# Kernel optimization log

Measured on AMD Instinct MI355X. Metric: run time of the kernel, lower is better.

Reference implementation:

```python
import jax, jax.numpy as jnp
import numpy as np
from jax import lax

B, S, F, H, V, T = 64, 1024, 128, 512, 64, 64
SOS, EOS = 0, 1


def lstm_cell(x, h, c, W_ih, W_hh, b_ih, b_hh):
    # PyTorch LSTM gate order: i, f, g, o
    gates = x @ W_ih.T + h @ W_hh.T + b_ih + b_hh  # [B, 4H]
    i, f, g, o = jnp.split(gates, 4, axis=-1)
    c_new = jax.nn.sigmoid(f) * c + jax.nn.sigmoid(i) * jnp.tanh(g)
    h_new = jax.nn.sigmoid(o) * jnp.tanh(c_new)
    return h_new, c_new


def setup_inputs() -> dict:
    key = jax.random.key(0)
    ks = jax.random.split(key, 12)
    s = 0.05  # weight scale to avoid gate saturation
    return {
        "signal": jax.random.normal(ks[0], (B, S, F), jnp.float32),
        "target": jax.random.randint(ks[1], (B, T), 0, V),
        "enc_W_ih": jax.random.normal(ks[2], (4 * H, F), jnp.float32) * s,
        "enc_W_hh": jax.random.normal(ks[3], (4 * H, H), jnp.float32) * s,
        "enc_b_ih": jax.random.normal(ks[4], (4 * H,), jnp.float32) * s,
        "enc_b_hh": jax.random.normal(ks[5], (4 * H,), jnp.float32) * s,
        "dec_W_ih": jax.random.normal(ks[6], (4 * H, V), jnp.float32) * s,
        "dec_W_hh": jax.random.normal(ks[7], (4 * H, H), jnp.float32) * s,
        "dec_b_ih": jax.random.normal(ks[8], (4 * H,), jnp.float32) * s,
        "dec_b_hh": jax.random.normal(ks[9], (4 * H,), jnp.float32) * s,
        "out_W": jax.random.normal(ks[10], (V, H), jnp.float32) * s,
        "out_b": jax.random.normal(ks[11], (V,), jnp.float32) * s,
    }


def reference(signal, target, enc_W_ih, enc_W_hh, enc_b_ih, enc_b_hh,
              dec_W_ih, dec_W_hh, dec_b_ih, dec_b_hh, out_W, out_b):
    b = signal.shape[0]
    hdim = enc_W_hh.shape[1]
    vocab = out_b.shape[0]
    n_steps = target.shape[1]  # max_loop = target.size(1)

    # ---- encoder LSTM (only final hidden state is used downstream) ----
    def enc_step(carry, x_t):
        h, c = carry
        h, c = lstm_cell(x_t, h, c, enc_W_ih, enc_W_hh, enc_b_ih, enc_b_hh)
        return (h, c), None

    h0 = jnp.zeros((b, hdim), signal.dtype)
    (h, c), _ = lax.scan(enc_step, (h0, h0), jnp.swapaxes(signal, 0, 1))

    # ---- decoder: teacher-start (one-hot target[:,0]) then greedy feedback ----
    inp0 = jax.nn.one_hot(target[:, 0], vocab, dtype=signal.dtype)  # [B, V]

    def dec_step(carry, _):
        h, c, x = carry
        x = jax.nn.relu(x)  # F.relu on one-hot input (faithful to source)
        h, c = lstm_cell(x, h, c, dec_W_ih, dec_W_hh, dec_b_ih, dec_b_hh)
        logits = h @ out_W.T + out_b  # [B, V]
        nxt = jax.nn.one_hot(jnp.argmax(logits, axis=-1), vocab, dtype=x.dtype)
        return (h, c, nxt), logits

    (_, _, _), logits = lax.scan(dec_step, (h, c, inp0), None, length=n_steps)
    logits = jnp.swapaxes(logits, 0, 1)  # [B, T, V]
    return jax.nn.log_softmax(logits, axis=-1)
```

## Files before the change

kernel.cpp:

```cpp
#include <hip/hip_runtime.h>
#include <cstddef>
#include <math.h>

#define NGROUP 4
#define WPG    32
#define NWG    128
#define BPG    16
#define BB  64
#define HH  512
#define TT  64
#define VV  64
#define FF  128
#define SS  1024

typedef _Float16 f16;
typedef _Float16 f16x8 __attribute__((ext_vector_type(8)));
typedef float    f32x4 __attribute__((ext_vector_type(4)));
typedef unsigned int u32;
typedef u32 u32x2 __attribute__((ext_vector_type(2)));
typedef u32 u32x4 __attribute__((ext_vector_type(4)));
typedef unsigned long long u64;

#define C1 4.8828125e-4f
#define C2 2.384185791015625e-7f

__device__ __forceinline__ void split8(const float* __restrict__ p, f16x8& hi, f16x8& lo) {
  f32x4 u = *(const f32x4*)p;
  f32x4 v = *(const f32x4*)(p + 4);
#pragma unroll
  for (int j = 0; j < 4; ++j) {
    f16 a = (f16)u[j]; hi[j]   = a; lo[j]   = (f16)((u[j] - (float)a) * 2048.0f);
    f16 b = (f16)v[j]; hi[4+j] = b; lo[4+j] = (f16)((v[j] - (float)b) * 2048.0f);
  }
}
__device__ __forceinline__ float sigmf_(float x) { return 1.0f / (1.0f + expf(-x)); }

__device__ __forceinline__ f32x4 ld16f(const void* p) {
  f32x4 r;
  asm volatile("global_load_dwordx4 %0, %1, off sc0 sc1" : "=v"(r) : "v"(p) : "memory");
  return r;
}
__device__ __forceinline__ void st4f(u32* p, u32 v) {
  __hip_atomic_store(p, v, __ATOMIC_RELAXED, __HIP_MEMORY_SCOPE_AGENT);
}
__device__ __forceinline__ void st4ff(float* p, float v) {
  __hip_atomic_store(p, v, __ATOMIC_RELAXED, __HIP_MEMORY_SCOPE_AGENT);
}
__device__ __forceinline__ u32 ld4f(const u32* p) {
  return __hip_atomic_load(p, __ATOMIC_RELAXED, __HIP_MEMORY_SCOPE_AGENT);
}
#define VMWAIT asm volatile("s_waitcnt vmcnt(0)" ::: "memory")

__device__ __forceinline__ void wait_flags(const u32* flags, u32 target, int lane) {
  const u32* a = flags + (size_t)(lane & 31) * 32;
  while (!__all(ld4f(a) >= target))
    __builtin_amdgcn_s_sleep(1);
}

#define MFMA(d, a, b) d = __builtin_amdgcn_mfma_f32_16x16x32_f16(a, b, d, 0, 0, 0)

#define STAGE_H(src_)                                                         \
  { const u32* src = (src_) + (size_t)(tid >> 4) * HH;                        \
    const int cq_ = tid & 15;                                                 \
    f32x4 sv[8];                                                              \
    _Pragma("unroll") for (int u2 = 0; u2 < 8; ++u2)                          \
      sv[u2] = ld16f(src + cq_*4 + u2*64);                                    \
    VMWAIT;                                                                   \
    _Pragma("unroll") for (int u2 = 0; u2 < 8; ++u2)                          \
      asm volatile("" : "+v"(sv[u2]));                                        \
    __builtin_amdgcn_sched_barrier(0);                                        \
    const int r_ = tid >> 4;                                                  \
    const size_t swz = (size_t)((r_ & 7) << 4);                               \
    _Pragma("unroll") for (int u2 = 0; u2 < 8; ++u2) {                        \
      union { f32x4 f; u32 u4[4]; } U; U.f = sv[u2];                          \
      u32 h0_ = (U.u4[0] & 0xffffu) | (U.u4[1] << 16);                        \
      u32 h1_ = (U.u4[2] & 0xffffu) | (U.u4[3] << 16);                        \
      u32 l0_ = (U.u4[0] >> 16) | (U.u4[1] & 0xffff0000u);                    \
      u32 l1_ = (U.u4[2] >> 16) | (U.u4[3] & 0xffff0000u);                    \
      size_t off = ((size_t)r_*1024 + (size_t)cq_*8 + (size_t)u2*128) ^ swz;  \
      *(u32x2*)((char*)sh_hi + off) = (u32x2){h0_, h1_};                      \
      *(u32x2*)((char*)sh_lo + off) = (u32x2){l0_, l1_};                      \
    } }                                                                       \
  __syncthreads();

#define LDA(s, ah, al)                                                        \
  { size_t o_ = ((size_t)mn * 1024 + (size_t)(s) * 64 + (size_t)(q8 * 2))     \
                ^ (size_t)((mn & 7) << 4);                                    \
    ah = *(const f16x8*)((const char*)sh_hi + o_);                            \
    al = *(const f16x8*)((const char*)sh_lo + o_); }

#define HPART()                                                               \
  _Pragma("unroll") for (int s = 0; s < 16; ++s) {                            \
    f16x8 ah, al; LDA(s, ah, al);                                             \
    MFMA(acc0, ah, whh_h[s]);                                                 \
    MFMA(acc1, al, whh_h[s]);                                                 \
    MFMA(acc1, ah, whh_l[s]);                                                 \
    MFMA(acc2, al, whh_l[s]);                                                 \
  }

#define GWRITE()                                                              \
  _Pragma("unroll") for (int r = 0; r < 4; ++r)                               \
    gate_buf[w][q * 4 + r][mn] = acc0[r] + C1 * acc1[r] + C2 * acc2[r];

__global__ void __launch_bounds__(256, 1) lstm_seq2seq(
    const float* __restrict__ sig,
    const int*   __restrict__ tgt,
    const float* __restrict__ eWih,
    const float* __restrict__ eWhh,
    const float* __restrict__ eBih,
    const float* __restrict__ eBhh,
    const float* __restrict__ dWih,
    const float* __restrict__ dWhh,
    const float* __restrict__ dBih,
    const float* __restrict__ dBhh,
    const float* __restrict__ oW,
    const float* __restrict__ oB,
    float*       __restrict__ out,
    unsigned char* __restrict__ ws)
{
  const int wg = blockIdx.x;
  const int g  = wg >> 5;
  const int p  = wg & 31;
  const int gb = g * BPG;
  u32* fl     = (u32*)ws + (size_t)g * 1024;
  u32* idxbuf = (u32*)(ws + 16384);
  u32* h16[2] = { (u32*)(ws + 20480) + (size_t)(g*2 + 0) * 8192,
                  (u32*)(ws + 20480) + (size_t)(g*2 + 1) * 8192 };
  float* hfg  = (float*)(ws + 282624) + (size_t)g * 8192;

  const int tid  = threadIdx.x;
  const int w    = tid >> 6;
  const int lane = tid & 63;
  const int q    = lane >> 4;
  const int mn   = lane & 15;
  const int q8   = q * 8;
  const int row  = w * HH + p * 16 + mn;
  const int cb   = tid >> 4;
  const int ck   = tid & 15;
  const int crow = p * 16 + ck;

  __shared__ __attribute__((aligned(16))) f16 sh_hi[16 * 512];
  __shared__ __attribute__((aligned(16))) f16 sh_lo[16 * 512];
  __shared__ float gate_buf[4][16][17];
  __shared__ float bias_buf[4][16];
  __shared__ __attribute__((aligned(16))) float hrow[512];
  __shared__ double psum[64];

  f16x8 whh_h[16], whh_l[16], wih_h[4], wih_l[4];
#pragma unroll
  for (int s = 0; s < 16; ++s)
    split8(eWhh + (size_t)row * HH + s * 32 + q8, whh_h[s], whh_l[s]);
#pragma unroll
  for (int s = 0; s < 4; ++s)
    split8(eWih + (size_t)row * FF + s * 32 + q8, wih_h[s], wih_l[s]);
  if (tid < 64) {
    int g4 = tid >> 4, kl = tid & 15;
    int r = g4 * HH + p * 16 + kl;
    bias_buf[g4][kl] = eBih[r] + eBhh[r];
  }
  if (p == 0 && tid < BPG)
    st4f(idxbuf + gb + tid, (u32)tgt[(size_t)(gb + tid) * TT]);
  __syncthreads();

  float c_reg = 0.f;
  int cur = 0;
  const f32x4 zero4 = {0.f, 0.f, 0.f, 0.f};

  for (int t = 0; t < SS; ++t) {
    f32x4 acc0 = zero4, acc1 = zero4, acc2 = zero4;
    const float* sb = sig + (size_t)(gb + mn) * (SS * FF) + (size_t)t * FF;
#pragma unroll
    for (int s = 0; s < 4; ++s) {
      f16x8 ah, al;
      split8(sb + s * 32 + q8, ah, al);
      MFMA(acc0, ah, wih_h[s]);
      MFMA(acc1, al, wih_h[s]);
      MFMA(acc1, ah, wih_l[s]);
      MFMA(acc2, al, wih_l[s]);
    }
    wait_flags(fl, (u32)t, lane);
    STAGE_H(h16[cur])
    HPART()
    GWRITE()
    __syncthreads();
    {
      float gi = gate_buf[0][cb][ck] + bias_buf[0][ck];
      float gf = gate_buf[1][cb][ck] + bias_buf[1][ck];
      float gg = gate_buf[2][cb][ck] + bias_buf[2][ck];
      float go = gate_buf[3][cb][ck] + bias_buf[3][ck];
      float c  = sigmf_(gf) * c_reg + sigmf_(gi) * tanhf(gg);
      float h  = sigmf_(go) * tanhf(c);
      c_reg = c;
      f16 hh = (f16)h;
      f16 hl = (f16)((h - (float)hh) * 2048.0f);
      union { f16 h2[2]; u32 u; } pk;
      pk.h2[0] = hh; pk.h2[1] = hl;
      st4f(h16[cur ^ 1] + (size_t)cb * HH + crow, pk.u);
    }
    VMWAIT;
    __syncthreads();
    if (tid == 0) st4f(fl + p * 32, (u32)(t + 1));
    cur ^= 1;
  }

#pragma unroll
  for (int s = 0; s < 16; ++s)
    split8(dWhh + (size_t)row * HH + s * 32 + q8, whh_h[s], whh_l[s]);
  __syncthreads();
  if (tid < 64) {
    int g4 = tid >> 4, kl = tid & 15;
    int r = g4 * HH + p * 16 + kl;
    bias_buf[g4][kl] = dBih[r] + dBhh[r];
  }
  __syncthreads();

  for (int t = 0; t < TT; ++t) {
    wait_flags(fl, (u32)(SS + 2 * t), lane);
    f32x4 acc0 = zero4, acc1 = zero4, acc2 = zero4;
    STAGE_H(h16[cur])
    HPART()
    GWRITE()
    __syncthreads();
    {
      int ib = (int)ld4f(idxbuf + gb + cb);
      float gi = gate_buf[0][cb][ck] + bias_buf[0][ck] + dWih[(size_t)(0*HH + crow) * VV + ib];
      float gf = gate_buf[1][cb][ck] + bias_buf[1][ck] + dWih[(size_t)(1*HH + crow) * VV + ib];
      float gg = gate_buf[2][cb][ck] + bias_buf[2][ck] + dWih[(size_t)(2*HH + crow) * VV + ib];
      float go = gate_buf[3][cb][ck] + bias_buf[3][ck] + dWih[(size_t)(3*HH + crow) * VV + ib];
      float c  = sigmf_(gf) * c_reg + sigmf_(gi) * tanhf(gg);
      float h  = sigmf_(go) * tanhf(c);
      c_reg = c;
      f16 hh = (f16)h;
      f16 hl = (f16)((h - (float)hh) * 2048.0f);
      union { f16 h2[2]; u32 u; } pk;
      pk.h2[0] = hh; pk.h2[1] = hl;
      st4f(h16[cur ^ 1] + (size_t)cb * HH + crow, pk.u);
      st4ff(hfg + (size_t)cb * HH + crow, h);
    }
    VMWAIT;
    __syncthreads();
    if (tid == 0) st4f(fl + p * 32, (u32)(SS + 2 * t + 1));
    int nxt = cur ^ 1;

    wait_flags(fl, (u32)(SS + 2 * t + 1), lane);
    if (p < BPG) {
      if (tid < 128) {
        f32x4 hv = ld16f(hfg + (size_t)p * HH + tid * 4);
        VMWAIT;
        *(f32x4*)&hrow[tid * 4] = hv;
      }
      __syncthreads();
      double acc = 0.0;
      if (w < 2) {
        const float* wr = oW + (size_t)lane * HH + w * 256;
        const float* hr = hrow + w * 256;
#pragma unroll 4
        for (int kc = 0; kc < 64; ++kc) {
          f32x4 hv = *(const f32x4*)(hr + kc * 4);
          f32x4 wv = *(const f32x4*)(wr + kc * 4);
          acc += (double)hv[0]*(double)wv[0] + (double)hv[1]*(double)wv[1]
               + (double)hv[2]*(double)wv[2] + (double)hv[3]*(double)wv[3];
        }
        if (w == 1) psum[lane] = acc;
      }
      __syncthreads();
      if (w == 0) {
        double l = acc + psum[lane] + (double)oB[lane];
        double mx = l; int ai = lane;
#pragma unroll
        for (int o = 32; o > 0; o >>= 1) {
          double om = __shfl_xor(mx, o, 64);
          int    oi = __shfl_xor(ai, o, 64);
          if (om > mx || (om == mx && oi < ai)) { mx = om; ai = oi; }
        }
        double se = exp(l - mx);
#pragma unroll
        for (int o = 32; o > 0; o >>= 1) se += __shfl_xor(se, o, 64);
        double lse = mx + log(se);
        out[((size_t)(gb + p) * TT + t) * VV + lane] = (float)(l - lse);
        if (lane == 0) st4f(idxbuf + gb + p, (u32)ai);
      }
    }
    VMWAIT;
    __syncthreads();
    if (tid == 0) st4f(fl + p * 32, (u32)(SS + 2 * t + 2));
    cur = nxt;
  }
}

extern "C" void kernel_launch(void* const* d_in, const int* in_sizes, int n_in,
                              void* d_out, int out_size, void* d_ws, size_t ws_size,
                              hipStream_t stream) {
  (void)in_sizes; (void)n_in; (void)out_size; (void)ws_size;
  hipMemsetAsync(d_ws, 0, 282624, stream);
  lstm_seq2seq<<<dim3(NWG), dim3(256), 0, stream>>>(
      (const float*)d_in[0],  (const int*)d_in[1],
      (const float*)d_in[2],  (const float*)d_in[3],
      (const float*)d_in[4],  (const float*)d_in[5],
      (const float*)d_in[6],  (const float*)d_in[7],
      (const float*)d_in[8],  (const float*)d_in[9],
      (const float*)d_in[10], (const float*)d_in[11],
      (float*)d_out, (unsigned char*)d_ws);
}
```

Before: 5.351 ms.

## Exchange hidden state as single fp16 and prefetch next input projection

The hidden state is now passed between workgroups as one fp16 value instead of an fp16 hi/lo pair. This halves the global exchange buffer, the LDS staging, and the recurrent MFMA count per step. The input-projection MFMAs for step t+1 are issued right after the h store of step t, so they overlap with the flag barrier wait instead of sitting on the critical path. The cost is lower precision in the recurrent h·W_hh product, which could drift over 1024 encoder steps and flip decoder argmax choices.

```diff
diff --git a/kernel.cpp b/kernel.cpp
--- a/kernel.cpp
+++ b/kernel.cpp
@@ -17,7 +17,6 @@
 typedef _Float16 f16x8 __attribute__((ext_vector_type(8)));
 typedef float    f32x4 __attribute__((ext_vector_type(4)));
 typedef unsigned int u32;
-typedef u32 u32x2 __attribute__((ext_vector_type(2)));
 typedef u32 u32x4 __attribute__((ext_vector_type(4)));
 typedef unsigned long long u64;
 
@@ -60,47 +59,57 @@
 #define MFMA(d, a, b) d = __builtin_amdgcn_mfma_f32_16x16x32_f16(a, b, d, 0, 0, 0)
 
 #define STAGE_H(src_)                                                         \
-  { const u32* src = (src_) + (size_t)(tid >> 4) * HH;                        \
+  { const u32* src = (src_) + (size_t)(tid >> 4) * 256;                       \
     const int cq_ = tid & 15;                                                 \
-    f32x4 sv[8];                                                              \
-    _Pragma("unroll") for (int u2 = 0; u2 < 8; ++u2)                          \
+    f32x4 sv[4];                                                              \
+    _Pragma("unroll") for (int u2 = 0; u2 < 4; ++u2)                          \
       sv[u2] = ld16f(src + cq_*4 + u2*64);                                    \
     VMWAIT;                                                                   \
-    _Pragma("unroll") for (int u2 = 0; u2 < 8; ++u2)                          \
+    _Pragma("unroll") for (int u2 = 0; u2 < 4; ++u2)                          \
       asm volatile("" : "+v"(sv[u2]));                                        \
     __builtin_amdgcn_sched_barrier(0);                                        \
     const int r_ = tid >> 4;                                                  \
     const size_t swz = (size_t)((r_ & 7) << 4);                               \
-    _Pragma("unroll") for (int u2 = 0; u2 < 8; ++u2) {                        \
-      union { f32x4 f; u32 u4[4]; } U; U.f = sv[u2];                          \
-      u32 h0_ = (U.u4[0] & 0xffffu) | (U.u4[1] << 16);                        \
-      u32 h1_ = (U.u4[2] & 0xffffu) | (U.u4[3] << 16);                        \
-      u32 l0_ = (U.u4[0] >> 16) | (U.u4[1] & 0xffff0000u);                    \
-      u32 l1_ = (U.u4[2] >> 16) | (U.u4[3] & 0xffff0000u);                    \
-      size_t off = ((size_t)r_*1024 + (size_t)cq_*8 + (size_t)u2*128) ^ swz;  \
-      *(u32x2*)((char*)sh_hi + off) = (u32x2){h0_, h1_};                      \
-      *(u32x2*)((char*)sh_lo + off) = (u32x2){l0_, l1_};                      \
+    _Pragma("unroll") for (int u2 = 0; u2 < 4; ++u2) {                        \
+      size_t off = ((size_t)r_*1024 + (size_t)cq_*16 + (size_t)u2*256) ^ swz; \
+      *(u32x4*)((char*)sh_h + off) = __builtin_bit_cast(u32x4, sv[u2]);       \
     } }                                                                       \
   __syncthreads();
 
-#define LDA(s, ah, al)                                                        \
+#define LDA(s, ah)                                                            \
   { size_t o_ = ((size_t)mn * 1024 + (size_t)(s) * 64 + (size_t)(q8 * 2))     \
                 ^ (size_t)((mn & 7) << 4);                                    \
-    ah = *(const f16x8*)((const char*)sh_hi + o_);                            \
-    al = *(const f16x8*)((const char*)sh_lo + o_); }
+    ah = *(const f16x8*)((const char*)sh_h + o_); }
 
 #define HPART()                                                               \
   _Pragma("unroll") for (int s = 0; s < 16; ++s) {                            \
-    f16x8 ah, al; LDA(s, ah, al);                                             \
+    f16x8 ah; LDA(s, ah);                                                     \
     MFMA(acc0, ah, whh_h[s]);                                                 \
-    MFMA(acc1, al, whh_h[s]);                                                 \
     MFMA(acc1, ah, whh_l[s]);                                                 \
-    MFMA(acc2, al, whh_l[s]);                                                 \
-  }
+  }
+
+#define XPART(ts)                                                             \
+  { acc0 = zero4; acc1 = zero4; acc2 = zero4;                                 \
+    const float* sb = sig + (size_t)(gb + mn) * (SS * FF) + (size_t)(ts) * FF;\
+    _Pragma("unroll") for (int s = 0; s < 4; ++s) {                           \
+      f16x8 xh, xl;                                                           \
+      split8(sb + s * 32 + q8, xh, xl);                                       \
+      MFMA(acc0, xh, wih_h[s]);                                               \
+      MFMA(acc1, xl, wih_h[s]);                                               \
+      MFMA(acc1, xh, wih_l[s]);                                               \
+      MFMA(acc2, xl, wih_l[s]);                                               \
+    } }
 
 #define GWRITE()                                                              \
   _Pragma("unroll") for (int r = 0; r < 4; ++r)                               \
     gate_buf[w][q * 4 + r][mn] = acc0[r] + C1 * acc1[r] + C2 * acc2[r];
+
+#define HSTORE(dst)                                                           \
+  { f16 hh = (f16)h;                                                          \
+    u32 mine = (u32)__builtin_bit_cast(unsigned short, hh);                   \
+    u32 part = (u32)__shfl_xor((int)mine, 1, 64);                             \
+    if ((tid & 1) == 0)                                                       \
+      st4f((dst) + (size_t)cb * 256 + p * 8 + (ck >> 1), mine | (part << 16)); }
 
 __global__ void __launch_bounds__(256, 1) lstm_seq2seq(
     const float* __restrict__ sig,
@@ -124,9 +133,9 @@
   const int gb = g * BPG;
   u32* fl     = (u32*)ws + (size_t)g * 1024;
   u32* idxbuf = (u32*)(ws + 16384);
-  u32* h16[2] = { (u32*)(ws + 20480) + (size_t)(g*2 + 0) * 8192,
-                  (u32*)(ws + 20480) + (size_t)(g*2 + 1) * 8192 };
-  float* hfg  = (float*)(ws + 282624) + (size_t)g * 8192;
+  u32* h16[2] = { (u32*)(ws + 20480) + (size_t)(g*2 + 0) * 4096,
+                  (u32*)(ws + 20480) + (size_t)(g*2 + 1) * 4096 };
+  float* hfg  = (float*)(ws + 151552) + (size_t)g * 8192;
 
   const int tid  = threadIdx.x;
   const int w    = tid >> 6;
@@ -139,8 +148,7 @@
   const int ck   = tid & 15;
   const int crow = p * 16 + ck;
 
-  __shared__ __attribute__((aligned(16))) f16 sh_hi[16 * 512];
-  __shared__ __attribute__((aligned(16))) f16 sh_lo[16 * 512];
+  __shared__ __attribute__((aligned(16))) f16 sh_h[16 * 512];
   __shared__ float gate_buf[4][16][17];
   __shared__ float bias_buf[4][16];
   __shared__ __attribute__((aligned(16))) float hrow[512];
@@ -165,19 +173,10 @@
   float c_reg = 0.f;
   int cur = 0;
   const f32x4 zero4 = {0.f, 0.f, 0.f, 0.f};
-
+  f32x4 acc0, acc1, acc2;
+
+  XPART(0)
   for (int t = 0; t < SS; ++t) {
-    f32x4 acc0 = zero4, acc1 = zero4, acc2 = zero4;
-    const float* sb = sig + (size_t)(gb + mn) * (SS * FF) + (size_t)t * FF;
-#pragma unroll
-    for (int s = 0; s < 4; ++s) {
-      f16x8 ah, al;
-      split8(sb + s * 32 + q8, ah, al);
-      MFMA(acc0, ah, wih_h[s]);
-      MFMA(acc1, al, wih_h[s]);
-      MFMA(acc1, ah, wih_l[s]);
-      MFMA(acc2, al, wih_l[s]);
-    }
     wait_flags(fl, (u32)t, lane);
     STAGE_H(h16[cur])
     HPART()
@@ -191,12 +190,9 @@
       float c  = sigmf_(gf) * c_reg + sigmf_(gi) * tanhf(gg);
       float h  = sigmf_(go) * tanhf(c);
       c_reg = c;
-      f16 hh = (f16)h;
-      f16 hl = (f16)((h - (float)hh) * 2048.0f);
-      union { f16 h2[2]; u32 u; } pk;
-      pk.h2[0] = hh; pk.h2[1] = hl;
-      st4f(h16[cur ^ 1] + (size_t)cb * HH + crow, pk.u);
+      HSTORE(h16[cur ^ 1])
     }
+    XPART(t + 1 < SS ? t + 1 : SS - 1)
     VMWAIT;
     __syncthreads();
     if (tid == 0) st4f(fl + p * 32, (u32)(t + 1));
@@ -216,7 +212,7 @@
 
   for (int t = 0; t < TT; ++t) {
     wait_flags(fl, (u32)(SS + 2 * t), lane);
-    f32x4 acc0 = zero4, acc1 = zero4, acc2 = zero4;
+    acc0 = zero4; acc1 = zero4; acc2 = zero4;
     STAGE_H(h16[cur])
     HPART()
     GWRITE()
@@ -230,11 +226,7 @@
       float c  = sigmf_(gf) * c_reg + sigmf_(gi) * tanhf(gg);
       float h  = sigmf_(go) * tanhf(c);
       c_reg = c;
-      f16 hh = (f16)h;
-      f16 hl = (f16)((h - (float)hh) * 2048.0f);
-      union { f16 h2[2]; u32 u; } pk;
-      pk.h2[0] = hh; pk.h2[1] = hl;
-      st4f(h16[cur ^ 1] + (size_t)cb * HH + crow, pk.u);
+      HSTORE(h16[cur ^ 1])
       st4ff(hfg + (size_t)cb * HH + crow, h);
     }
     VMWAIT;
@@ -292,7 +284,7 @@
                               void* d_out, int out_size, void* d_ws, size_t ws_size,
                               hipStream_t stream) {
   (void)in_sizes; (void)n_in; (void)out_size; (void)ws_size;
-  hipMemsetAsync(d_ws, 0, 282624, stream);
+  hipMemsetAsync(d_ws, 0, 151552, stream);
   lstm_seq2seq<<<dim3(NWG), dim3(256), 0, stream>>>(
       (const float*)d_in[0],  (const int*)d_in[1],
       (const float*)d_in[2],  (const float*)d_in[3],
```

Result: faster. 5.016 ms (-6.3%).
